# Kernel optimization log

Measured on AMD Instinct MI355X. Metric: run time of the kernel, lower is better.

The kernel has to match this reference:

```python
import jax, jax.numpy as jnp
import numpy as np

N_E = 1024      # codes per sub-codebook
E_DIM = 64      # code dimension
BETA = 0.25     # commitment cost (VectorQuantizer(n_e, e_dim, 0.25))


def setup_inputs() -> dict:
    key = jax.random.key(0)
    k1, k2 = jax.random.split(key)
    bs, c, h, w = 16, 512, 32, 32
    m = c // E_DIM  # 8 sub-codebooks
    z = jax.random.normal(k1, (bs, c, h, w), dtype=jnp.float32)
    # taming-style init: uniform(-1/n_e, 1/n_e)
    codebooks = jax.random.uniform(
        k2, (m, N_E, E_DIM), dtype=jnp.float32,
        minval=-1.0 / N_E, maxval=1.0 / N_E)
    return {"z": z, "codebooks": codebooks}


def reference(z, codebooks):
    bs, c, h, w = z.shape
    m, n_e, e_dim = codebooks.shape
    N = bs * h * w
    # [bs,c,h,w] -> [bs,h,w,c] -> [m, N, e_dim]: batched over all m sub-codebooks at once
    zf = z.transpose(0, 2, 3, 1).reshape(N, m, e_dim).transpose(1, 0, 2)

    # squared L2 distances: ||z||^2 + ||e||^2 - 2 z.e   -> [m, N, n_e]
    d = ((zf ** 2).sum(-1, keepdims=True)
         + (codebooks ** 2).sum(-1)[:, None, :]
         - 2.0 * jnp.einsum('mnd,mkd->mnk', zf, codebooks))
    idx = jnp.argmin(d, axis=-1)  # [m, N]

    # gather nearest codes: [m, N, e_dim]
    zq = jnp.take_along_axis(codebooks, idx[:, :, None], axis=1)

    # per-sub-codebook VQ loss, summed over m (loss = sum(loss_list))
    codebook_loss = jnp.mean((jax.lax.stop_gradient(zq) - zf) ** 2, axis=(1, 2))
    commit_loss = jnp.mean((zq - jax.lax.stop_gradient(zf)) ** 2, axis=(1, 2))
    loss = jnp.sum(codebook_loss + BETA * commit_loss)

    # straight-through estimator
    zq_st = zf + jax.lax.stop_gradient(zq - zf)

    # reassemble: [m,N,d] -> [N,m*d] -> [bs,h,w,c] -> [bs,c,h,w]
    z_vq = zq_st.transpose(1, 0, 2).reshape(bs, h, w, c).transpose(0, 3, 1, 2)

    # concat of per-codebook index tensors along dim 0
    min_encoding_indices = idx.reshape(-1)  # [m*N]
    # per-code occupancy counts summed over the m codebooks -> [n_e]
    bin_count = jnp.zeros((n_e,), jnp.int32).at[min_encoding_indices].add(1)

    return z_vq, loss, min_encoding_indices, bin_count
```

## Files before the change

kernel.cpp:

```cpp
#include <hip/hip_runtime.h>
#include <cfloat>

#define BS 16
#define CC 512
#define HWD 1024
#define NN 16384
#define MM 8
#define NE 1024
#define ED 64

#define LOSS_OFF 8388608
#define IDX_OFF  8388609
#define BIN_OFF  8519681

#define TAU 4e-5f
#define UWIN 400u

#define WS_B     0
#define WS_IDX   32768
#define WS_CNT   557056
#define WS_LIST  557088
#define WS_OF    688160
#define WS_CAND  720928
#define WS_BMAT  3866656

typedef __attribute__((ext_vector_type(8))) short bf16x8;
typedef __attribute__((ext_vector_type(16))) float f32x16;

__device__ __forceinline__ unsigned short f2bf(float f) {
    unsigned int u = __float_as_uint(f);
    unsigned int r = (u + 0x7fffu + ((u >> 16) & 1u)) >> 16;
    return (unsigned short)r;
}
__device__ __forceinline__ float bf2f(unsigned short h) {
    return __uint_as_float(((unsigned int)h) << 16);
}
__device__ __forceinline__ unsigned umin_(unsigned a, unsigned b) { return a < b ? a : b; }
__device__ __forceinline__ unsigned umax_(unsigned a, unsigned b) { return a > b ? a : b; }
__device__ __forceinline__ unsigned umin3(unsigned a, unsigned b, unsigned c) {
    return umin_(umin_(a, b), c);
}

__device__ __forceinline__ float mul_rn(float a, float b) {
#pragma clang fp contract(off)
    return a * b;
}
__device__ __forceinline__ float add_rn(float a, float b) {
#pragma clang fp contract(off)
    return a + b;
}
__device__ __forceinline__ float sub_rn(float a, float b) {
#pragma clang fp contract(off)
    return a - b;
}

__device__ __forceinline__ float np_sumsq64(const float* x) {
    float r[8];
#pragma unroll
    for (int j = 0; j < 8; ++j) r[j] = mul_rn(x[j], x[j]);
#pragma unroll
    for (int i = 8; i < 64; i += 8) {
#pragma unroll
        for (int j = 0; j < 8; ++j) r[j] = add_rn(r[j], mul_rn(x[i + j], x[i + j]));
    }
    return add_rn(add_rn(add_rn(r[0], r[1]), add_rn(r[2], r[3])),
                  add_rn(add_rn(r[4], r[5]), add_rn(r[6], r[7])));
}

__device__ __forceinline__ float np_dot64(const float* zsh, const float4* cr4) {
    float v0 = 0.f, v1 = 0.f, v2 = 0.f, v3 = 0.f;
#pragma unroll
    for (int t = 0; t < 4; ++t) {
        float4 e0 = cr4[t * 4 + 0];
        float4 e1 = cr4[t * 4 + 1];
        float4 e2 = cr4[t * 4 + 2];
        float4 e3 = cr4[t * 4 + 3];
        const int d0 = 16 * t;
        v0 = add_rn(mul_rn(zsh[d0 + 0], e0.x),
             add_rn(mul_rn(zsh[d0 + 4], e1.x),
             add_rn(mul_rn(zsh[d0 + 8], e2.x),
             add_rn(mul_rn(zsh[d0 + 12], e3.x), v0))));
        v1 = add_rn(mul_rn(zsh[d0 + 1], e0.y),
             add_rn(mul_rn(zsh[d0 + 5], e1.y),
             add_rn(mul_rn(zsh[d0 + 9], e2.y),
             add_rn(mul_rn(zsh[d0 + 13], e3.y), v1))));
        v2 = add_rn(mul_rn(zsh[d0 + 2], e0.z),
             add_rn(mul_rn(zsh[d0 + 6], e1.z),
             add_rn(mul_rn(zsh[d0 + 10], e2.z),
             add_rn(mul_rn(zsh[d0 + 14], e3.z), v2))));
        v3 = add_rn(mul_rn(zsh[d0 + 3], e0.w),
             add_rn(mul_rn(zsh[d0 + 7], e1.w),
             add_rn(mul_rn(zsh[d0 + 11], e2.w),
             add_rn(mul_rn(zsh[d0 + 15], e3.w), v3))));
    }
    return add_rn(add_rn(v0, v1), add_rn(v2, v3));
}

__global__ __launch_bounds__(256) void prep_kernel(const float* __restrict__ cb,
                                                   float* __restrict__ Bhat,
                                                   uint4* __restrict__ Bmat,
                                                   float* __restrict__ out,
                                                   int* __restrict__ cnt) {
    const int tid = threadIdx.x;
    if (blockIdx.x < 32) {
        int i = blockIdx.x * 256 + tid;
        if (i == 0) { out[LOSS_OFF] = 0.0f; cnt[0] = 0; cnt[1] = 0; }
        if (i < NE) out[BIN_OFF + i] = 0.0f;
        const float4* r4 = (const float4*)(cb + (size_t)i * ED);
        float x[ED];
#pragma unroll
        for (int q = 0; q < 16; ++q) {
            float4 v = r4[q];
            x[q*4+0] = v.x; x[q*4+1] = v.y; x[q*4+2] = v.z; x[q*4+3] = v.w;
        }
        Bhat[i] = np_sumsq64(x);
        return;
    }
    int t = (blockIdx.x - 32) * 256 + tid;
    int lane = t & 63;
    int ct = (t >> 6) & 31;
    int rem = t >> 11;
    int c = rem % 13;
    int m = rem / 13;
    int h = lane >> 5;
    int k = ct * 32 + (lane & 31);

    unsigned short v[8];
#pragma unroll
    for (int j = 0; j < 8; ++j) v[j] = 0;

    if (c < 12) {
        int d0 = 16 * (c & 3) + 8 * h;
        const float* e = cb + ((size_t)m * NE + k) * ED + d0;
#pragma unroll
        for (int j = 0; j < 8; ++j) {
            float f = -2.0f * e[j];
            unsigned short hi = f2bf(f);
            v[j] = (c >= 4 && c < 8) ? f2bf(f - bf2f(hi)) : hi;
        }
    } else if (h == 0) {
        const float* e = cb + ((size_t)m * NE + k) * ED;
        float s = 0.f;
#pragma unroll
        for (int d = 0; d < ED; ++d) s += e[d] * e[d];
        v[0] = f2bf(s);
        v[1] = 0x3F80;
    }
    uint4 o;
    o.x = (unsigned)v[0] | ((unsigned)v[1] << 16);
    o.y = (unsigned)v[2] | ((unsigned)v[3] << 16);
    o.z = (unsigned)v[4] | ((unsigned)v[5] << 16);
    o.w = (unsigned)v[6] | ((unsigned)v[7] << 16);
    Bmat[t] = o;
}

__global__ __launch_bounds__(512, 4) void argmin_kernel(
        const float* __restrict__ z, const uint4* __restrict__ Bmat,
        int* __restrict__ idx_out, int* __restrict__ cnt,
        int* __restrict__ list, unsigned short* __restrict__ cand) {
    const int tid = threadIdx.x;
    const int m = blockIdx.y;
    const int row0 = blockIdx.x * 256;
    const int w = tid >> 6;
    const int l = tid & 63;
    const int h = l >> 5;
    const int r5 = l & 31;

    __shared__ uint4 ldsB[3][13 * 2 * 64];

    const int n_mine = row0 + w * 32 + r5;
    const int b = n_mine >> 10;
    const int hw = n_mine & (HWD - 1);
    const float* zbase = z + (((size_t)(b * CC + m * ED)) << 10) + hw;

    bf16x8 zh[4], zl[4];
#pragma unroll
    for (int i = 0; i < 4; ++i) {
        int o = 2 * i + h;
#pragma unroll
        for (int j = 0; j < 8; ++j) {
            float f = zbase[(size_t)(8 * o + j) << 10];
            unsigned short hb = f2bf(f);
            unsigned short lb = f2bf(f - bf2f(hb));
            zh[i][j] = (short)hb;
            zl[i][j] = (short)lb;
        }
    }
    bf16x8 ones12 = {0, 0, 0, 0, 0, 0, 0, 0};
    if (h == 0) { ones12[0] = (short)0x3F80; ones12[1] = (short)0x3F80; }

    unsigned rbm = 0xFFFFFFF0u, rsec = 0xFFFFFFFFu, rinfo = 0;
    int ccnt = 0;
    unsigned cq0 = 0, cq1 = 0, cq2 = 0;
    auto push = [&](unsigned id) {
        cq2 = (cq2 << 16) | (cq1 >> 16);
        cq1 = (cq1 << 16) | (cq0 >> 16);
        cq0 = (cq0 << 16) | (id & 0xFFFFu);
        ccnt++;
    };

    auto stage = [&](int g, int bufi) {
        for (int seg = w; seg < 26; seg += 8) {
            int c = seg >> 1, ct2 = seg & 1;
            const uint4* src = Bmat +
                ((size_t)((m * 13 + c) * 32 + (g * 2 + ct2)) << 6) + l;
            uint4* dst = &ldsB[bufi][(c * 2 + ct2) * 64];
            __builtin_amdgcn_global_load_lds(
                (const __attribute__((address_space(1))) unsigned int*)src,
                (__attribute__((address_space(3))) unsigned int*)dst, 16, 0, 0);
        }
    };

    stage(0, 0);
    stage(1, 1);
    asm volatile("s_waitcnt vmcnt(3)" ::: "memory");
    __builtin_amdgcn_s_barrier();

    int bR = 0;
    for (int g = 0; g < 16; ++g) {
        int bW = bR + 2; if (bW >= 3) bW -= 3;
        if (g < 14) stage(g + 2, bW);
        const uint4* Bb = &ldsB[bR][0];

#pragma unroll
        for (int ctl = 0; ctl < 2; ++ctl) {
            f32x16 acc;
#pragma unroll
            for (int s = 0; s < 16; ++s) acc[s] = 0.0f;
#pragma unroll
            for (int c = 0; c < 13; ++c) {
                bf16x8 af = *(const bf16x8*)&Bb[(c * 2 + ctl) * 64 + l];
                bf16x8 bfr = (c < 8) ? zh[c & 3] : ((c < 12) ? zl[c & 3] : ones12);
                acc = __builtin_amdgcn_mfma_f32_32x32x16_bf16(af, bfr, acc, 0, 0, 0);
            }
            unsigned u[16];
#pragma unroll
            for (int s = 0; s < 16; ++s)
                u[s] = (__float_as_uint(acc[s]) & 0xFFFFFFF0u) | (unsigned)s;
            unsigned b0 = umin_(u[0], u[1]),  s0 = umax_(u[0], u[1]);
            unsigned b1 = umin_(u[2], u[3]),  s1 = umax_(u[2], u[3]);
            unsigned b2 = umin_(u[4], u[5]),  s2 = umax_(u[4], u[5]);
            unsigned b3 = umin_(u[6], u[7]),  s3 = umax_(u[6], u[7]);
            unsigned b4 = umin_(u[8], u[9]),  s4 = umax_(u[8], u[9]);
            unsigned b5 = umin_(u[10], u[11]), s5 = umax_(u[10], u[11]);
            unsigned b6 = umin_(u[12], u[13]), s6 = umax_(u[12], u[13]);
            unsigned b7 = umin_(u[14], u[15]), s7 = umax_(u[14], u[15]);
            unsigned B0 = umin_(b0, b1), S0 = umin3(umax_(b0, b1), s0, s1);
            unsigned B1 = umin_(b2, b3), S1 = umin3(umax_(b2, b3), s2, s3);
            unsigned B2 = umin_(b4, b5), S2 = umin3(umax_(b4, b5), s4, s5);
            unsigned B3 = umin_(b6, b7), S3 = umin3(umax_(b6, b7), s6, s7);
            unsigned C0 = umin_(B0, B1), T0 = umin3(umax_(B0, B1), S0, S1);
            unsigned C1 = umin_(B2, B3), T1 = umin3(umax_(B2, B3), S2, S3);
            unsigned bt = umin_(C0, C1), st = umin3(umax_(C0, C1), T0, T1);

            unsigned tile = (unsigned)(g * 2 + ctl);
            unsigned oldrbm = rbm;
            bool take = bt < oldrbm;
            unsigned newrbm = take ? bt : oldrbm;
            unsigned limit = newrbm + UWIN;
            rsec = umin3(rsec, st, take ? oldrbm : bt);
            int sbt = (int)(bt & 15u);
            if (take) {
                if (bt + UWIN < oldrbm) ccnt = 0;
                push(tile * 32u + ((unsigned)sbt & 3u) +
                     8u * ((unsigned)sbt >> 2) + 4u * (unsigned)h);
                rinfo = (tile << 4) | (unsigned)sbt;
            }
            rbm = newrbm;
            unsigned gatev = take ? st : bt;
            if (gatev < limit) {
#pragma unroll
                for (int s = 0; s < 16; ++s) {
                    if (u[s] < limit && !(take && s == sbt))
                        push(tile * 32u + ((unsigned)s & 3u) +
                             8u * ((unsigned)s >> 2) + 4u * (unsigned)h);
                }
            }
        }

        if (g < 14) {
            asm volatile("s_waitcnt vmcnt(3)" ::: "memory");
        } else if (g == 14) {
            asm volatile("s_waitcnt vmcnt(0)" ::: "memory");
        }
        if (g < 15) __builtin_amdgcn_s_barrier();
        bR = (bR == 2) ? 0 : bR + 1;
    }

    unsigned short* myslots = cand + ((size_t)(m * NN + n_mine) * 2 + h) * 6;
    if (ccnt) {
        unsigned* cp = (unsigned*)myslots;
        cp[0] = cq0; cp[1] = cq1; cp[2] = cq2;
    }

    int pcnt = __shfl_xor(ccnt, 32, 64);

    unsigned ss = rinfo & 15u, tile = rinfo >> 4;
    int k = (int)(tile * 32 + (ss & 3u) + 8u * (ss >> 2) + 4u * (unsigned)h);
    unsigned orbm = __shfl_xor(rbm, 32, 64);
    int ok = __shfl_xor(k, 32, 64);
    unsigned orsec = __shfl_xor(rsec, 32, 64);
    bool take = orbm < rbm;
    unsigned lose = take ? rbm : orbm;
    unsigned fb = take ? orbm : rbm;
    int fk = take ? ok : k;
    unsigned fs = umin3(rsec, orsec, lose);
    if (l < 32) {
        int mn = m * NN + n_mine;
        idx_out[mn] = fk;
        float margin = __uint_as_float(fs & 0xFFFFFFF0u) -
                       __uint_as_float(fb & 0xFFFFFFF0u);
        if (margin < TAU) {
            int p = atomicAdd(cnt, 1);
            if (p < 32768) {
                int c0 = ccnt > 6 ? 7 : ccnt;
                int c1 = pcnt > 6 ? 7 : pcnt;
                list[p] = mn | (c0 << 20) | (c1 << 24);
            }
        }
    }
}

__global__ __launch_bounds__(256) void cand_kernel(
        const float* __restrict__ z, const float* __restrict__ cb,
        const float* __restrict__ Bhat, int* __restrict__ cnt,
        const int* __restrict__ list, const unsigned short* __restrict__ cand,
        int* __restrict__ idx_out, int* __restrict__ oflist) {
    const int tid = threadIdx.x;
    const int lane = tid & 63;
    const int wv = tid >> 6;
    const int wid = (blockIdx.x * 256 + tid) >> 6;
    const int nw = gridDim.x * 4;
    const int total = cnt[0] < 32768 ? cnt[0] : 32768;

    __shared__ float zsh[4][ED];

    for (int r = wid; r < total; r += nw) {
        const int e = list[r];
        const int mn = e & 0xFFFFF;
        const int c0 = (e >> 20) & 15;
        const int c1 = (e >> 24) & 15;
        if (c0 == 7 || c1 == 7) {
            if (lane == 0) {
                int q = atomicAdd(cnt + 1, 1);
                if (q < 8192) oflist[q] = mn;
            }
            continue;
        }
        const int m = mn >> 14;
        const int n = mn & (NN - 1);
        const int b = n >> 10;
        const int hw = n & (HWD - 1);

        zsh[wv][lane] = z[(((size_t)(b * CC + m * ED + lane)) << 10) + hw];

        int kj = -1;
        if (lane < c0) kj = cand[(size_t)mn * 12 + lane];
        else if (lane >= 8 && lane < 8 + c1) kj = cand[(size_t)mn * 12 + 6 + (lane - 8)];

        float A = np_sumsq64(&zsh[wv][0]);

        float dref = FLT_MAX;
        if (kj >= 0) {
            const float4* cr4 = (const float4*)(cb + ((size_t)m * NE + kj) * ED);
            float C = np_dot64(&zsh[wv][0], cr4);
            dref = sub_rn(add_rn(A, Bhat[m * NE + kj]), mul_rn(2.0f, C));
        }
        int kk = (kj >= 0) ? kj : NE;
#pragma unroll
        for (int off = 32; off >= 1; off >>= 1) {
            float ov = __shfl_down(dref, off, 64);
            int oi = __shfl_down(kk, off, 64);
            if (ov < dref || (ov == dref && oi < kk)) { dref = ov; kk = oi; }
        }
        if (lane == 0) idx_out[mn] = kk;
    }
}

__global__ __launch_bounds__(256) void emul_kernel(
        const float* __restrict__ z, const float* __restrict__ cb,
        const float* __restrict__ Bhat, const int* __restrict__ cnt,
        const int* __restrict__ oflist, int* __restrict__ idx_out) {
    const int tid = threadIdx.x;
    const int lane = tid & 63;
    const int w = tid >> 6;
    const int total = cnt[1] < 8192 ? cnt[1] : 8192;

    __shared__ float zsh[ED];
    __shared__ float rbest[4];
    __shared__ int ridx[4];

    for (int r = blockIdx.x; r < total; r += gridDim.x) {
        const int mn = oflist[r];
        const int m = mn >> 14;
        const int n = mn & (NN - 1);
        const int b = n >> 10;
        const int hw = n & (HWD - 1);

        __syncthreads();
        if (tid < ED) {
            const float* zbase = z + (((size_t)(b * CC + m * ED)) << 10) + hw;
            zsh[tid] = zbase[(size_t)tid << 10];
        }
        __syncthreads();

        const float A = np_sumsq64(zsh);
        const float* cbm = cb + (size_t)m * NE * ED;
        const float* Bm = Bhat + m * NE;
        float best = FLT_MAX;
        int bidx = NE;
#pragma unroll
        for (int kk = 0; kk < 4; ++kk) {
            const int k = kk * 256 + tid;
            const float4* cr4 = (const float4*)(cbm + (size_t)k * ED);
            float C = np_dot64(zsh, cr4);
            float dk = sub_rn(add_rn(A, Bm[k]), mul_rn(2.0f, C));
            if (dk < best || (dk == best && k < bidx)) { best = dk; bidx = k; }
        }
#pragma unroll
        for (int off = 32; off >= 1; off >>= 1) {
            float ov = __shfl_down(best, off, 64);
            int oi = __shfl_down(bidx, off, 64);
            if (ov < best || (ov == best && oi < bidx)) { best = ov; bidx = oi; }
        }
        if (lane == 0) { rbest[w] = best; ridx[w] = bidx; }
        __syncthreads();
        if (tid == 0) {
            float bb = rbest[0]; int bi = ridx[0];
#pragma unroll
            for (int i = 1; i < 4; ++i) {
                if (rbest[i] < bb || (rbest[i] == bb && ridx[i] < bi)) {
                    bb = rbest[i]; bi = ridx[i];
                }
            }
            idx_out[mn] = bi;
        }
    }
}

__global__ __launch_bounds__(256) void output_kernel(
        const float* __restrict__ z, const float* __restrict__ cb,
        const int* __restrict__ idx_in, float* __restrict__ out) {
    const int tid = threadIdx.x;
    const int n = blockIdx.x * 256 + tid;
    const int m = blockIdx.y;
    const int b = n >> 10;
    const int hw = n & (HWD - 1);
    const int idx = idx_in[m * NN + n];

    out[IDX_OFF + m * NN + n] = (float)idx;

    const float* cr = cb + ((size_t)m * NE + (size_t)idx) * ED;
    const float* zbase = z + (((size_t)(b * CC + m * ED)) << 10) + hw;
    float* ob = out + (((size_t)(b * CC + m * ED)) << 10) + hw;

    double acc = 0.0;
#pragma unroll
    for (int d = 0; d < ED; ++d) {
        float c = cr[d];
        float zv = zbase[(size_t)d << 10];
        ob[(size_t)d << 10] = c;
        float diff = c - zv;
        acc += (double)diff * (double)diff;
    }

    __shared__ int hist[NE];
#pragma unroll
    for (int i = 0; i < 4; ++i) hist[tid + i * 256] = 0;
    __syncthreads();
    atomicAdd(&hist[idx], 1);

#pragma unroll
    for (int off = 32; off >= 1; off >>= 1)
        acc += __shfl_down(acc, off, 64);
    __shared__ double wsum[4];
    if ((tid & 63) == 0) wsum[tid >> 6] = acc;
    __syncthreads();
    if (tid == 0) {
        double t = wsum[0] + wsum[1] + wsum[2] + wsum[3];
        atomicAdd(out + LOSS_OFF, (float)(t * (1.25 / 1048576.0)));
    }
#pragma unroll
    for (int i = 0; i < 4; ++i) {
        int v = hist[tid + i * 256];
        if (v) atomicAdd(out + BIN_OFF + tid + i * 256, (float)v);
    }
}

extern "C" void kernel_launch(void* const* d_in, const int* in_sizes, int n_in,
                              void* d_out, int out_size, void* d_ws, size_t ws_size,
                              hipStream_t stream) {
    const float* z = (const float*)d_in[0];
    const float* cb = (const float*)d_in[1];
    float* out = (float*)d_out;
    char* ws = (char*)d_ws;
    float* Bhat = (float*)(ws + WS_B);
    int* idxw = (int*)(ws + WS_IDX);
    int* cnt = (int*)(ws + WS_CNT);
    int* list = (int*)(ws + WS_LIST);
    int* oflist = (int*)(ws + WS_OF);
    unsigned short* cand = (unsigned short*)(ws + WS_CAND);
    uint4* Bmat = (uint4*)(ws + WS_BMAT);

    prep_kernel<<<dim3(864), dim3(256), 0, stream>>>(cb, Bhat, Bmat, out, cnt);
    argmin_kernel<<<dim3(NN / 256, MM), dim3(512), 0, stream>>>(
        z, Bmat, idxw, cnt, list, cand);
    cand_kernel<<<dim3(256), dim3(256), 0, stream>>>(
        z, cb, Bhat, cnt, list, cand, idxw, oflist);
    emul_kernel<<<dim3(256), dim3(256), 0, stream>>>(
        z, cb, Bhat, cnt, oflist, idxw);
    output_kernel<<<dim3(NN / 256, MM), dim3(256), 0, stream>>>(z, cb, idxw, out);
}
```

Measured before the change: 175.5 us.

## Process two row groups per wave to reuse codebook fragments across MFMAs

New measurement: 178.8 us. No clear change (+1.8%).

```diff
diff --git a/kernel.cpp b/kernel.cpp
--- a/kernel.cpp
+++ b/kernel.cpp
@@ -154,7 +154,7 @@
     Bmat[t] = o;
 }
 
-__global__ __launch_bounds__(512, 4) void argmin_kernel(
+__global__ __launch_bounds__(256, 2) void argmin_kernel(
         const float* __restrict__ z, const uint4* __restrict__ Bmat,
         int* __restrict__ idx_out, int* __restrict__ cnt,
         int* __restrict__ list, unsigned short* __restrict__ cand) {
@@ -168,39 +168,42 @@
 
     __shared__ uint4 ldsB[3][13 * 2 * 64];
 
-    const int n_mine = row0 + w * 32 + r5;
-    const int b = n_mine >> 10;
-    const int hw = n_mine & (HWD - 1);
-    const float* zbase = z + (((size_t)(b * CC + m * ED)) << 10) + hw;
-
-    bf16x8 zh[4], zl[4];
+    const int n0 = row0 + w * 64 + r5;
+    const int n1 = n0 + 32;
+    const int b = n0 >> 10;
+    const int hw0 = n0 & (HWD - 1);
+    const float* zbase0 = z + (((size_t)(b * CC + m * ED)) << 10) + hw0;
+    const float* zbase1 = zbase0 + 32;
+
+    bf16x8 zh0[4], zl0[4], zh1[4], zl1[4];
 #pragma unroll
     for (int i = 0; i < 4; ++i) {
         int o = 2 * i + h;
 #pragma unroll
         for (int j = 0; j < 8; ++j) {
-            float f = zbase[(size_t)(8 * o + j) << 10];
+            float f = zbase0[(size_t)(8 * o + j) << 10];
             unsigned short hb = f2bf(f);
             unsigned short lb = f2bf(f - bf2f(hb));
-            zh[i][j] = (short)hb;
-            zl[i][j] = (short)lb;
+            zh0[i][j] = (short)hb;
+            zl0[i][j] = (short)lb;
+            float g = zbase1[(size_t)(8 * o + j) << 10];
+            unsigned short hb1 = f2bf(g);
+            unsigned short lb1 = f2bf(g - bf2f(hb1));
+            zh1[i][j] = (short)hb1;
+            zl1[i][j] = (short)lb1;
         }
     }
     bf16x8 ones12 = {0, 0, 0, 0, 0, 0, 0, 0};
     if (h == 0) { ones12[0] = (short)0x3F80; ones12[1] = (short)0x3F80; }
 
-    unsigned rbm = 0xFFFFFFF0u, rsec = 0xFFFFFFFFu, rinfo = 0;
-    int ccnt = 0;
-    unsigned cq0 = 0, cq1 = 0, cq2 = 0;
-    auto push = [&](unsigned id) {
-        cq2 = (cq2 << 16) | (cq1 >> 16);
-        cq1 = (cq1 << 16) | (cq0 >> 16);
-        cq0 = (cq0 << 16) | (id & 0xFFFFu);
-        ccnt++;
-    };
+    unsigned rbm0 = 0xFFFFFFF0u, rsec0 = 0xFFFFFFFFu, rinfo0 = 0;
+    unsigned rbm1 = 0xFFFFFFF0u, rsec1 = 0xFFFFFFFFu, rinfo1 = 0;
+    int ccnt0 = 0, ccnt1 = 0;
+    unsigned q00 = 0, q01 = 0, q02 = 0;
+    unsigned q10 = 0, q11 = 0, q12 = 0;
 
     auto stage = [&](int g, int bufi) {
-        for (int seg = w; seg < 26; seg += 8) {
+        for (int seg = w; seg < 26; seg += 4) {
             int c = seg >> 1, ct2 = seg & 1;
             const uint4* src = Bmat +
                 ((size_t)((m * 13 + c) * 32 + (g * 2 + ct2)) << 6) + l;
@@ -211,9 +214,65 @@
         }
     };
 
+    auto process = [&](const f32x16& acc, unsigned tile,
+                       unsigned& rbm, unsigned& rsec, unsigned& rinfo, int& ccnt,
+                       unsigned& cq0, unsigned& cq1, unsigned& cq2) {
+        unsigned u[16];
+#pragma unroll
+        for (int s = 0; s < 16; ++s)
+            u[s] = (__float_as_uint(acc[s]) & 0xFFFFFFF0u) | (unsigned)s;
+        unsigned b0 = umin_(u[0], u[1]),  s0 = umax_(u[0], u[1]);
+        unsigned b1 = umin_(u[2], u[3]),  s1 = umax_(u[2], u[3]);
+        unsigned b2 = umin_(u[4], u[5]),  s2 = umax_(u[4], u[5]);
+        unsigned b3 = umin_(u[6], u[7]),  s3 = umax_(u[6], u[7]);
+        unsigned b4 = umin_(u[8], u[9]),  s4 = umax_(u[8], u[9]);
+        unsigned b5 = umin_(u[10], u[11]), s5 = umax_(u[10], u[11]);
+        unsigned b6 = umin_(u[12], u[13]), s6 = umax_(u[12], u[13]);
+        unsigned b7 = umin_(u[14], u[15]), s7 = umax_(u[14], u[15]);
+        unsigned B0 = umin_(b0, b1), S0 = umin3(umax_(b0, b1), s0, s1);
+        unsigned B1 = umin_(b2, b3), S1 = umin3(umax_(b2, b3), s2, s3);
+        unsigned B2 = umin_(b4, b5), S2 = umin3(umax_(b4, b5), s4, s5);
+        unsigned B3 = umin_(b6, b7), S3 = umin3(umax_(b6, b7), s6, s7);
+        unsigned C0 = umin_(B0, B1), T0 = umin3(umax_(B0, B1), S0, S1);
+        unsigned C1 = umin_(B2, B3), T1 = umin3(umax_(B2, B3), S2, S3);
+        unsigned bt = umin_(C0, C1), st = umin3(umax_(C0, C1), T0, T1);
+
+        unsigned oldrbm = rbm;
+        bool take = bt < oldrbm;
+        unsigned newrbm = take ? bt : oldrbm;
+        unsigned limit = newrbm + UWIN;
+        rsec = umin3(rsec, st, take ? oldrbm : bt);
+        int sbt = (int)(bt & 15u);
+        if (take) {
+            if (bt + UWIN < oldrbm) ccnt = 0;
+            unsigned id = tile * 32u + ((unsigned)sbt & 3u) +
+                          8u * ((unsigned)sbt >> 2) + 4u * (unsigned)h;
+            cq2 = (cq2 << 16) | (cq1 >> 16);
+            cq1 = (cq1 << 16) | (cq0 >> 16);
+            cq0 = (cq0 << 16) | (id & 0xFFFFu);
+            ccnt++;
+            rinfo = (tile << 4) | (unsigned)sbt;
+        }
+        rbm = newrbm;
+        unsigned gatev = take ? st : bt;
+        if (gatev < limit) {
+#pragma unroll
+            for (int s = 0; s < 16; ++s) {
+                if (u[s] < limit && !(take && s == sbt)) {
+                    unsigned id = tile * 32u + ((unsigned)s & 3u) +
+                                  8u * ((unsigned)s >> 2) + 4u * (unsigned)h;
+                    cq2 = (cq2 << 16) | (cq1 >> 16);
+                    cq1 = (cq1 << 16) | (cq0 >> 16);
+                    cq0 = (cq0 << 16) | (id & 0xFFFFu);
+                    ccnt++;
+                }
+            }
+        }
+    };
+
     stage(0, 0);
     stage(1, 1);
-    asm volatile("s_waitcnt vmcnt(3)" ::: "memory");
+    asm volatile("s_waitcnt vmcnt(6)" ::: "memory");
     __builtin_amdgcn_s_barrier();
 
     int bR = 0;
@@ -224,101 +283,76 @@
 
 #pragma unroll
         for (int ctl = 0; ctl < 2; ++ctl) {
-            f32x16 acc;
-#pragma unroll
-            for (int s = 0; s < 16; ++s) acc[s] = 0.0f;
+            f32x16 a0, a1;
+#pragma unroll
+            for (int s = 0; s < 16; ++s) { a0[s] = 0.0f; a1[s] = 0.0f; }
+            __builtin_amdgcn_s_setprio(1);
 #pragma unroll
             for (int c = 0; c < 13; ++c) {
                 bf16x8 af = *(const bf16x8*)&Bb[(c * 2 + ctl) * 64 + l];
-                bf16x8 bfr = (c < 8) ? zh[c & 3] : ((c < 12) ? zl[c & 3] : ones12);
-                acc = __builtin_amdgcn_mfma_f32_32x32x16_bf16(af, bfr, acc, 0, 0, 0);
+                bf16x8 z0 = (c < 8) ? zh0[c & 3] : ((c < 12) ? zl0[c & 3] : ones12);
+                bf16x8 z1 = (c < 8) ? zh1[c & 3] : ((c < 12) ? zl1[c & 3] : ones12);
+                a0 = __builtin_amdgcn_mfma_f32_32x32x16_bf16(af, z0, a0, 0, 0, 0);
+                a1 = __builtin_amdgcn_mfma_f32_32x32x16_bf16(af, z1, a1, 0, 0, 0);
             }
-            unsigned u[16];
-#pragma unroll
-            for (int s = 0; s < 16; ++s)
-                u[s] = (__float_as_uint(acc[s]) & 0xFFFFFFF0u) | (unsigned)s;
-            unsigned b0 = umin_(u[0], u[1]),  s0 = umax_(u[0], u[1]);
-            unsigned b1 = umin_(u[2], u[3]),  s1 = umax_(u[2], u[3]);
-            unsigned b2 = umin_(u[4], u[5]),  s2 = umax_(u[4], u[5]);
-            unsigned b3 = umin_(u[6], u[7]),  s3 = umax_(u[6], u[7]);
-            unsigned b4 = umin_(u[8], u[9]),  s4 = umax_(u[8], u[9]);
-            unsigned b5 = umin_(u[10], u[11]), s5 = umax_(u[10], u[11]);
-            unsigned b6 = umin_(u[12], u[13]), s6 = umax_(u[12], u[13]);
-            unsigned b7 = umin_(u[14], u[15]), s7 = umax_(u[14], u[15]);
-            unsigned B0 = umin_(b0, b1), S0 = umin3(umax_(b0, b1), s0, s1);
-            unsigned B1 = umin_(b2, b3), S1 = umin3(umax_(b2, b3), s2, s3);
-            unsigned B2 = umin_(b4, b5), S2 = umin3(umax_(b4, b5), s4, s5);
-            unsigned B3 = umin_(b6, b7), S3 = umin3(umax_(b6, b7), s6, s7);
-            unsigned C0 = umin_(B0, B1), T0 = umin3(umax_(B0, B1), S0, S1);
-            unsigned C1 = umin_(B2, B3), T1 = umin3(umax_(B2, B3), S2, S3);
-            unsigned bt = umin_(C0, C1), st = umin3(umax_(C0, C1), T0, T1);
-
+            __builtin_amdgcn_s_setprio(0);
             unsigned tile = (unsigned)(g * 2 + ctl);
-            unsigned oldrbm = rbm;
-            bool take = bt < oldrbm;
-            unsigned newrbm = take ? bt : oldrbm;
-            unsigned limit = newrbm + UWIN;
-            rsec = umin3(rsec, st, take ? oldrbm : bt);
-            int sbt = (int)(bt & 15u);
-            if (take) {
-                if (bt + UWIN < oldrbm) ccnt = 0;
-                push(tile * 32u + ((unsigned)sbt & 3u) +
-                     8u * ((unsigned)sbt >> 2) + 4u * (unsigned)h);
-                rinfo = (tile << 4) | (unsigned)sbt;
-            }
-            rbm = newrbm;
-            unsigned gatev = take ? st : bt;
-            if (gatev < limit) {
-#pragma unroll
-                for (int s = 0; s < 16; ++s) {
-                    if (u[s] < limit && !(take && s == sbt))
-                        push(tile * 32u + ((unsigned)s & 3u) +
-                             8u * ((unsigned)s >> 2) + 4u * (unsigned)h);
+            process(a0, tile, rbm0, rsec0, rinfo0, ccnt0, q00, q01, q02);
+            process(a1, tile, rbm1, rsec1, rinfo1, ccnt1, q10, q11, q12);
+        }
+
+        if (g < 14) {
+            asm volatile("s_waitcnt vmcnt(6)" ::: "memory");
+        } else if (g == 14) {
+            asm volatile("s_waitcnt vmcnt(0)" ::: "memory");
+        }
+        if (g < 15) __builtin_amdgcn_s_barrier();
+        bR = (bR == 2) ? 0 : bR + 1;
+    }
+
+    {
+        unsigned short* s0 = cand + ((size_t)(m * NN + n0) * 2 + h) * 6;
+        if (ccnt0) {
+            unsigned* cp = (unsigned*)s0;
+            cp[0] = q00; cp[1] = q01; cp[2] = q02;
+        }
+        unsigned short* s1 = cand + ((size_t)(m * NN + n1) * 2 + h) * 6;
+        if (ccnt1) {
+            unsigned* cp = (unsigned*)s1;
+            cp[0] = q10; cp[1] = q11; cp[2] = q12;
+        }
+    }
+
+    auto finish = [&](unsigned rbm, unsigned rsec, unsigned rinfo, int ccnt,
+                      int n_mine) {
+        int pcnt = __shfl_xor(ccnt, 32, 64);
+        unsigned ss = rinfo & 15u, tile = rinfo >> 4;
+        int k = (int)(tile * 32 + (ss & 3u) + 8u * (ss >> 2) + 4u * (unsigned)h);
+        unsigned orbm = __shfl_xor(rbm, 32, 64);
+        int ok = __shfl_xor(k, 32, 64);
+        unsigned orsec = __shfl_xor(rsec, 32, 64);
+        bool take = orbm < rbm;
+        unsigned lose = take ? rbm : orbm;
+        unsigned fb = take ? orbm : rbm;
+        int fk = take ? ok : k;
+        unsigned fs = umin3(rsec, orsec, lose);
+        if (l < 32) {
+            int mn = m * NN + n_mine;
+            idx_out[mn] = fk;
+            float margin = __uint_as_float(fs & 0xFFFFFFF0u) -
+                           __uint_as_float(fb & 0xFFFFFFF0u);
+            if (margin < TAU) {
+                int p = atomicAdd(cnt, 1);
+                if (p < 32768) {
+                    int c0 = ccnt > 6 ? 7 : ccnt;
+                    int c1 = pcnt > 6 ? 7 : pcnt;
+                    list[p] = mn | (c0 << 20) | (c1 << 24);
                 }
             }
         }
-
-        if (g < 14) {
-            asm volatile("s_waitcnt vmcnt(3)" ::: "memory");
-        } else if (g == 14) {
-            asm volatile("s_waitcnt vmcnt(0)" ::: "memory");
-        }
-        if (g < 15) __builtin_amdgcn_s_barrier();
-        bR = (bR == 2) ? 0 : bR + 1;
-    }
-
-    unsigned short* myslots = cand + ((size_t)(m * NN + n_mine) * 2 + h) * 6;
-    if (ccnt) {
-        unsigned* cp = (unsigned*)myslots;
-        cp[0] = cq0; cp[1] = cq1; cp[2] = cq2;
-    }
-
-    int pcnt = __shfl_xor(ccnt, 32, 64);
-
-    unsigned ss = rinfo & 15u, tile = rinfo >> 4;
-    int k = (int)(tile * 32 + (ss & 3u) + 8u * (ss >> 2) + 4u * (unsigned)h);
-    unsigned orbm = __shfl_xor(rbm, 32, 64);
-    int ok = __shfl_xor(k, 32, 64);
-    unsigned orsec = __shfl_xor(rsec, 32, 64);
-    bool take = orbm < rbm;
-    unsigned lose = take ? rbm : orbm;
-    unsigned fb = take ? orbm : rbm;
-    int fk = take ? ok : k;
-    unsigned fs = umin3(rsec, orsec, lose);
-    if (l < 32) {
-        int mn = m * NN + n_mine;
-        idx_out[mn] = fk;
-        float margin = __uint_as_float(fs & 0xFFFFFFF0u) -
-                       __uint_as_float(fb & 0xFFFFFFF0u);
-        if (margin < TAU) {
-            int p = atomicAdd(cnt, 1);
-            if (p < 32768) {
-                int c0 = ccnt > 6 ? 7 : ccnt;
-                int c1 = pcnt > 6 ? 7 : pcnt;
-                list[p] = mn | (c0 << 20) | (c1 << 24);
-            }
-        }
-    }
+    };
+    finish(rbm0, rsec0, rinfo0, ccnt0, n0);
+    finish(rbm1, rsec1, rinfo1, ccnt1, n1);
 }
 
 __global__ __launch_bounds__(256) void cand_kernel(
@@ -503,7 +537,7 @@
     uint4* Bmat = (uint4*)(ws + WS_BMAT);
 
     prep_kernel<<<dim3(864), dim3(256), 0, stream>>>(cb, Bhat, Bmat, out, cnt);
-    argmin_kernel<<<dim3(NN / 256, MM), dim3(512), 0, stream>>>(
+    argmin_kernel<<<dim3(NN / 256, MM), dim3(256), 0, stream>>>(
         z, Bmat, idxw, cnt, list, cand);
     cand_kernel<<<dim3(256), dim3(256), 0, stream>>>(
         z, cb, Bhat, cnt, list, cand, idxw, oflist);
```
